# Kernel tuning notes

Hardware: AMD Instinct MI355X
Metric: run time of the kernel (lower is better)

Reference implementation:

```python
import jax, jax.numpy as jnp
import numpy as np

PSP_SIZES = (1, 3, 6, 8)  # KV length S = 1 + 9 + 36 + 64 = 110
BN_EPS = 1e-5


def conv1x1(x, W, b):
    # x: [B,C,H,W], W: [O,C], b: [O] -> [B,O,H,W]
    return jnp.einsum('bchw,oc->bohw', x, W) + b[None, :, None, None]


def psp(f):
    # f: [B,C,H,W] -> [B,C,S]; H,W divisible by all sizes so adaptive pool == block mean
    B, C, H, W = f.shape
    priors = []
    for s in PSP_SIZES:
        p = f.reshape(B, C, s, H // s, s, W // s).mean(axis=(3, 5))  # [B,C,s,s]
        priors.append(p.reshape(B, C, s * s))
    return jnp.concatenate(priors, axis=-1)  # [B,C,S]


def setup_inputs() -> dict:
    key = jax.random.key(0)
    ks = jax.random.split(key, 8)
    B, C, H, W = 8, 512, 72, 72
    Kc, Vc = 256, 256
    return {
        'x': jax.random.normal(ks[0], (B, C, H, W), jnp.float32),
        'Wk': jax.random.normal(ks[1], (Kc, C), jnp.float32) * (1.0 / np.sqrt(C)),
        'bk': jax.random.normal(ks[2], (Kc,), jnp.float32) * 0.01,
        'gamma': jnp.ones((Kc,), jnp.float32),
        'beta': jnp.zeros((Kc,), jnp.float32),
        'rmean': jnp.zeros((Kc,), jnp.float32),
        'rvar': jax.random.uniform(ks[3], (Kc,), jnp.float32, 0.5, 1.5),
        'Wv': jax.random.normal(ks[4], (Vc, C), jnp.float32) * (1.0 / np.sqrt(C)),
        'bv': jax.random.normal(ks[5], (Vc,), jnp.float32) * 0.01,
        'Ww': jax.random.normal(ks[6], (C, Vc), jnp.float32) * (1.0 / np.sqrt(Vc)),
        'bw': jnp.zeros((C,), jnp.float32),
    }


def reference(x, Wk, bk, gamma, beta, rmean, rvar, Wv, bv, Ww, bw):
    B, C, H, W = x.shape
    Kc = Wk.shape[0]
    Vc = Wv.shape[0]
    # f_value: conv1x1, then PSP -> value [B,S,Vc]
    value = psp(conv1x1(x, Wv, bv)).transpose(0, 2, 1)
    # f_key == f_query: conv1x1 + BN(inference) + ReLU
    k = conv1x1(x, Wk, bk)
    inv = gamma / jnp.sqrt(rvar + BN_EPS)
    k = jax.nn.relu(k * inv[None, :, None, None] + (beta - rmean * inv)[None, :, None, None])
    query = k.reshape(B, Kc, H * W).transpose(0, 2, 1)  # [B,HW,Kc]
    keyt = psp(k)  # [B,Kc,S]
    sim = jnp.einsum('bnk,bks->bns', query, keyt) * (Kc ** -0.5)
    sim = jax.nn.softmax(sim, axis=-1)
    context = jnp.einsum('bns,bsv->bnv', sim, value)  # [B,HW,Vc]
    context = context.transpose(0, 2, 1).reshape(B, Vc, H, W)
    return conv1x1(context, Ww, bw)
```

## Files before the change

kernel.cpp:

```cpp
#include <hip/hip_runtime.h>
#include <hip/hip_bf16.h>

#define HW    5184
#define WIDTH 72
#define CIN   512
#define KC    256
#define VC    256
#define NS    110
#define NSP   112
#define SPV   128
#define BATCH 8

typedef unsigned short u16;
typedef unsigned int   u32;
typedef __attribute__((ext_vector_type(8))) short bf16x8;
typedef __attribute__((ext_vector_type(4))) float f32x4;

typedef const __attribute__((address_space(1))) u32* gp_t;
typedef __attribute__((address_space(3))) u32* lp_t;

__device__ __forceinline__ u32 f2bf1(float f) {
    u32 u = __float_as_uint(f);
    return (u + 0x7FFFu + ((u >> 16) & 1u)) >> 16;
}
__device__ __forceinline__ u32 pack2(float a, float b) {
    return f2bf1(a) | (f2bf1(b) << 16);
}

__global__ void prep_kernel(const float* __restrict__ bk, const float* __restrict__ gamma,
                            const float* __restrict__ beta, const float* __restrict__ rmean,
                            const float* __restrict__ rvar, float* __restrict__ inv_out,
                            float* __restrict__ bc_out) {
    int i = threadIdx.x;
    float inv = gamma[i] * rsqrtf(rvar[i] + 1e-5f);
    inv_out[i] = inv;
    bc_out[i]  = bk[i] * inv + beta[i] - rmean[i] * inv;
}

__global__ __launch_bounds__(256) void cvt_w_kernel(
    const float* __restrict__ Wk, const float* __restrict__ Ww, const float* __restrict__ Wv,
    u16* __restrict__ Wkbf, u16* __restrict__ Wwbf, u16* __restrict__ Wvbf)
{
    int j = (blockIdx.x * 256 + threadIdx.x) * 4;
    const float* s; u16* d;
    if (j < KC * CIN)          { s = Wk; d = Wkbf; }
    else if (j < 2 * KC * CIN) { j -= KC * CIN;     s = Ww; d = Wwbf; }
    else                       { j -= 2 * KC * CIN; s = Wv; d = Wvbf; }
    float4 v = *(const float4*)&s[j];
    uint2 u;
    u.x = pack2(v.x, v.y);
    u.y = pack2(v.z, v.w);
    *(uint2*)&d[j] = u;
}

__global__ __launch_bounds__(256) void transpose_cvt_kernel(
    const float* __restrict__ in, u16* __restrict__ out, int C)
{
    const int z  = blockIdx.z;
    const int n0 = blockIdx.x * 32;
    const int k0 = blockIdx.y * 32;
    __shared__ float t[32][33];
    const int tx = threadIdx.x & 31, ty = threadIdx.x >> 5;
    const float* src = in + ((size_t)z * C + k0) * HW + n0;
#pragma unroll
    for (int i = 0; i < 4; i++)
        t[ty + i * 8][tx] = src[(size_t)(ty + i * 8) * HW + tx];
    __syncthreads();
    u16* dst = out + ((size_t)z * HW + n0) * C + k0;
    const int kp  = (threadIdx.x & 15) * 2;
    const int nl0 = threadIdx.x >> 4;
#pragma unroll
    for (int j = 0; j < 2; j++) {
        int nl = nl0 + j * 16;
        u32 u = pack2(t[kp][nl], t[kp + 1][nl]);
        *(u32*)&dst[(size_t)nl * C + kp] = u;
    }
}

__global__ __launch_bounds__(256) void gemm_nt_bf16(
    const u16* __restrict__ A, const u16* __restrict__ B, float* __restrict__ C,
    u16* __restrict__ Ct,
    int M, int N, int K, int nbx, int nby,
    const float* __restrict__ scale, const float* __restrict__ bias, int relu)
{
    const int tot = nbx * nby * BATCH;
    const int q = tot >> 3, r = tot & 7;
    const int xcd = blockIdx.x & 7;
    const int wg  = (xcd < r ? xcd * (q + 1) : r * (q + 1) + (xcd - r) * q) + (blockIdx.x >> 3);
    const int mb_ = wg % nby;
    const int nb_ = (wg / nby) % nbx;
    const int z   = wg / (nby * nbx);

    const int n0 = nb_ * 128;
    const int m0 = mb_ * 128;
    const size_t boff = (size_t)z * N * K;
    const size_t coff = (size_t)z * M * N;
    const int tid  = threadIdx.x;
    const int wid  = tid >> 6;
    const int lane = tid & 63;

    __shared__ __align__(16) u16 As[3][4][128][8];
    __shared__ __align__(16) u16 Bs[3][4][128][8];

    const int kg0  = (wid & 1) * 2;
    const int half = (wid >> 1) * 64;

    const u16* gA = A + (size_t)(m0 + half + lane) * K + kg0 * 8;
    int nIdx = n0 + half + lane;
    if (nIdx > N - 1) nIdx = N - 1;
    const u16* gB = B + boff + (size_t)nIdx * K + kg0 * 8;

    const int wm  = (wid >> 1) * 64;
    const int wn  = (wid & 1) * 64;
    const int l16 = lane & 15;
    const int lq  = lane >> 4;

    f32x4 acc[4][4];
#pragma unroll
    for (int mi = 0; mi < 4; mi++)
#pragma unroll
        for (int ni = 0; ni < 4; ni++)
            acc[mi][ni] = (f32x4){0.f, 0.f, 0.f, 0.f};

#define STAGE(d, kk)                                                                              \
    __builtin_amdgcn_global_load_lds((gp_t)(gA + (kk)),     (lp_t)&As[d][kg0][half][0], 16, 0, 0);\
    __builtin_amdgcn_global_load_lds((gp_t)(gA + (kk) + 8), (lp_t)&As[d][kg0+1][half][0],16, 0, 0);\
    __builtin_amdgcn_global_load_lds((gp_t)(gB + (kk)),     (lp_t)&Bs[d][kg0][half][0], 16, 0, 0);\
    __builtin_amdgcn_global_load_lds((gp_t)(gB + (kk) + 8), (lp_t)&Bs[d][kg0+1][half][0],16, 0, 0);

    const int NT = K >> 5;
    STAGE(0, 0)
    STAGE(1, 32)

    int cur = 0;
    for (int t = 0; t < NT; ++t) {
        if (t + 1 < NT) { asm volatile("s_waitcnt vmcnt(4)" ::: "memory"); }
        else            { asm volatile("s_waitcnt vmcnt(0)" ::: "memory"); }
        __builtin_amdgcn_s_barrier();
        __builtin_amdgcn_sched_barrier(0);

        if (t + 2 < NT) {
            int nb = cur + 2; if (nb >= 3) nb -= 3;
            STAGE(nb, (t + 2) * 32)
        }

        bf16x8 af[4], bf[4];
#pragma unroll
        for (int i = 0; i < 4; i++) {
            af[i] = *(const bf16x8*)&As[cur][lq][wm + i * 16 + l16][0];
            bf[i] = *(const bf16x8*)&Bs[cur][lq][wn + i * 16 + l16][0];
        }
        __builtin_amdgcn_s_setprio(1);
#pragma unroll
        for (int mi = 0; mi < 4; mi++)
#pragma unroll
            for (int ni = 0; ni < 4; ni++)
                acc[mi][ni] = __builtin_amdgcn_mfma_f32_16x16x32_bf16(
                    af[mi], bf[ni], acc[mi][ni], 0, 0, 0);
        __builtin_amdgcn_s_setprio(0);

        cur = (cur == 2) ? 0 : cur + 1;
    }
#undef STAGE

#pragma unroll
    for (int mi = 0; mi < 4; mi++) {
        const int mb = m0 + wm + mi * 16 + lq * 4;
        float sc[4], bi[4];
#pragma unroll
        for (int r2 = 0; r2 < 4; r2++) {
            sc[r2] = scale ? scale[mb + r2] : 1.0f;
            bi[r2] = bias  ? bias[mb + r2]  : 0.0f;
        }
#pragma unroll
        for (int ni = 0; ni < 4; ni++) {
            const int n = n0 + wn + ni * 16 + l16;
            if (n < N) {
                float v[4];
#pragma unroll
                for (int r2 = 0; r2 < 4; r2++) {
                    v[r2] = acc[mi][ni][r2] * sc[r2] + bi[r2];
                    if (relu) v[r2] = fmaxf(v[r2], 0.f);
                    C[coff + (size_t)(mb + r2) * N + n] = v[r2];
                }
                if (Ct) {
                    uint2 u;
                    u.x = pack2(v[0], v[1]);
                    u.y = pack2(v[2], v[3]);
                    *(uint2*)&Ct[(size_t)z * N * M + (size_t)n * M + mb] = u;
                }
            }
        }
    }
}

__global__ __launch_bounds__(256) void value_mfma_kernel(
    const u16* __restrict__ A, const u16* __restrict__ Bp,
    const float* __restrict__ bv, u16* __restrict__ valT)
{
    const int m0 = blockIdx.x * 128;
    const int b  = blockIdx.y;
    const int tid  = threadIdx.x;
    const int wid  = tid >> 6;
    const int lane = tid & 63;

    __shared__ __align__(16) u16 As[4][128][8];
    __shared__ __align__(16) u16 Bs[4][128][8];

    const int kg0  = (wid & 1) * 2;
    const int half = (wid >> 1) * 64;

    const u16* gA = A + (size_t)(m0 + half + lane) * CIN + kg0 * 8;
    const u16* gB = Bp + (size_t)b * SPV * CIN + (size_t)(half + lane) * CIN + kg0 * 8;

    lp_t lA0 = (lp_t)&As[kg0][half][0];
    lp_t lA1 = (lp_t)&As[kg0 + 1][half][0];
    lp_t lB0 = (lp_t)&Bs[kg0][half][0];
    lp_t lB1 = (lp_t)&Bs[kg0 + 1][half][0];

    const int wm  = (wid >> 1) * 64;
    const int wn  = (wid & 1) * 64;
    const int l16 = lane & 15;
    const int lq  = lane >> 4;

    f32x4 acc[4][4];
#pragma unroll
    for (int mi = 0; mi < 4; mi++)
#pragma unroll
        for (int ni = 0; ni < 4; ni++)
            acc[mi][ni] = (f32x4){0.f, 0.f, 0.f, 0.f};

    for (int k0 = 0; k0 < CIN; k0 += 32) {
        __builtin_amdgcn_global_load_lds((gp_t)(gA + k0),     lA0, 16, 0, 0);
        __builtin_amdgcn_global_load_lds((gp_t)(gA + k0 + 8), lA1, 16, 0, 0);
        __builtin_amdgcn_global_load_lds((gp_t)(gB + k0),     lB0, 16, 0, 0);
        __builtin_amdgcn_global_load_lds((gp_t)(gB + k0 + 8), lB1, 16, 0, 0);
        __syncthreads();

        bf16x8 af[4], bf[4];
#pragma unroll
        for (int i = 0; i < 4; i++) {
            af[i] = *(const bf16x8*)&As[lq][wm + i * 16 + l16][0];
            bf[i] = *(const bf16x8*)&Bs[lq][wn + i * 16 + l16][0];
        }
#pragma unroll
        for (int mi = 0; mi < 4; mi++)
#pragma unroll
            for (int ni = 0; ni < 4; ni++)
                acc[mi][ni] = __builtin_amdgcn_mfma_f32_16x16x32_bf16(
                    af[mi], bf[ni], acc[mi][ni], 0, 0, 0);
        __syncthreads();
    }

    char* vb = (char*)valT + (size_t)b * VC * SPV * 2;
#pragma unroll
    for (int mi = 0; mi < 4; mi++) {
        const int mb = m0 + wm + mi * 16 + lq * 4;
        float bi[4];
#pragma unroll
        for (int r = 0; r < 4; r++) bi[r] = bv[mb + r];
#pragma unroll
        for (int ni = 0; ni < 4; ni++) {
            const int n = wn + ni * 16 + l16;
#pragma unroll
            for (int r = 0; r < 4; r++) {
                const int v = mb + r;
                const int byte = v * 256 + ((n * 2) ^ ((v & 7) << 4));
                *(u16*)(vb + byte) = (u16)f2bf1(acc[mi][ni][r] + bi[r]);
            }
        }
    }
}

__global__ __launch_bounds__(128) void psp_pool_px_kernel(
    const float* __restrict__ in, u16* __restrict__ out)
{
    const int c = blockIdx.x;
    const int b = blockIdx.y;
    const int t = threadIdx.x;
    __shared__ float4 row4[1296];
    __shared__ float aux[100];
    float* row = (float*)row4;
    const float* src = in + ((size_t)b * CIN + c) * HW;
    for (int idx = t; idx < 1296; idx += 128)
        row4[idx] = *(const float4*)(src + idx * 4);
    __syncthreads();
    if (t < 64) {
        int r0 = (t >> 3) * 9, c0 = (t & 7) * 9;
        float s = 0.f;
        for (int i = 0; i < 9; i++)
            for (int j = 0; j < 9; j++) s += row[(r0 + i) * WIDTH + c0 + j];
        aux[t] = s;
    } else if (t < 100) {
        int tt = t - 64;
        int r0 = (tt / 6) * 12, c0 = (tt % 6) * 12;
        float s = 0.f;
        for (int i = 0; i < 12; i++)
            for (int j = 0; j < 12; j++) s += row[(r0 + i) * WIDTH + c0 + j];
        aux[64 + tt] = s;
    }
    __syncthreads();
    u16* ob = out + (size_t)b * SPV * CIN + c;
    if (t < 64) ob[(size_t)(46 + t) * CIN] = (u16)f2bf1(aux[t] * (1.f / 81.f));
    if (t < 36) ob[(size_t)(10 + t) * CIN] = (u16)f2bf1(aux[64 + t] * (1.f / 144.f));
    if (t < 9) {
        int r = t / 3, cc = t % 3;
        float s4 = aux[64 + (2 * r) * 6 + 2 * cc] + aux[64 + (2 * r) * 6 + 2 * cc + 1]
                 + aux[64 + (2 * r + 1) * 6 + 2 * cc] + aux[64 + (2 * r + 1) * 6 + 2 * cc + 1];
        ob[(size_t)(1 + t) * CIN] = (u16)f2bf1(s4 * (1.f / 576.f));
    }
    if (t == 0) {
        float s = 0.f;
        for (int i = 0; i < 64; i++) s += aux[i];
        ob[0] = (u16)f2bf1(s * (1.f / 5184.f));
    }
    if (t < 18) ob[(size_t)(110 + t) * CIN] = 0;
}

__global__ __launch_bounds__(128) void psp_pool_bf16_kernel(
    const float* __restrict__ in, u16* __restrict__ out)
{
    const int c = blockIdx.x;
    const int b = blockIdx.y;
    const int t = threadIdx.x;
    __shared__ float4 row4[1296];
    __shared__ float aux[100];
    float* row = (float*)row4;
    const float* src = in + ((size_t)b * KC + c) * HW;
    for (int idx = t; idx < 1296; idx += 128)
        row4[idx] = *(const float4*)(src + idx * 4);
    __syncthreads();
    if (t < 64) {
        int r0 = (t >> 3) * 9, c0 = (t & 7) * 9;
        float s = 0.f;
        for (int i = 0; i < 9; i++)
            for (int j = 0; j < 9; j++) s += row[(r0 + i) * WIDTH + c0 + j];
        aux[t] = s;
    } else if (t < 100) {
        int tt = t - 64;
        int r0 = (tt / 6) * 12, c0 = (tt % 6) * 12;
        float s = 0.f;
        for (int i = 0; i < 12; i++)
            for (int j = 0; j < 12; j++) s += row[(r0 + i) * WIDTH + c0 + j];
        aux[64 + tt] = s;
    }
    __syncthreads();
    char* ob = (char*)out + (size_t)b * NSP * KC * 2;
    const int c2 = c * 2;
#define KWR(S, V) *(u16*)(ob + (S) * 512 + (c2 ^ (((S) & 7) << 4))) = (u16)f2bf1(V)
    if (t < 64) KWR(46 + t, aux[t] * (1.f / 81.f));
    if (t < 36) KWR(10 + t, aux[64 + t] * (1.f / 144.f));
    if (t < 9) {
        int r = t / 3, cc = t % 3;
        float s4 = aux[64 + (2 * r) * 6 + 2 * cc] + aux[64 + (2 * r) * 6 + 2 * cc + 1]
                 + aux[64 + (2 * r + 1) * 6 + 2 * cc] + aux[64 + (2 * r + 1) * 6 + 2 * cc + 1];
        KWR(1 + t, s4 * (1.f / 576.f));
    }
    if (t == 0) {
        float s = 0.f;
        for (int i = 0; i < 64; i++) s += aux[i];
        KWR(0, s * (1.f / 5184.f));
        KWR(110, 0.f);
        KWR(111, 0.f);
    }
#undef KWR
}

__global__ __launch_bounds__(256) void attn_mfma_kernel(
    const u16* __restrict__ qT, const u16* __restrict__ keyt,
    const u16* __restrict__ valT, u16* __restrict__ ctxT)
{
    const int b    = blockIdx.y;
    const int tid  = threadIdx.x;
    const int wid  = tid >> 6;
    const int lane = tid & 63;
    const int l16  = lane & 15;
    const int lq   = lane >> 4;
    const int px0  = blockIdx.x * 64 + wid * 16;

    __shared__ __align__(16) u16 SM[61440];
    char* base = (char*)SM;
    const int VOFF = 57344;

    {
        const char* gk = (const char*)keyt + (size_t)b * (NSP * KC * 2);
        const char* gv = (const char*)valT + (size_t)b * (VC * SPV * 2);
#pragma unroll
        for (int i = 0; i < 14; i++) {
            const int o = (wid * 14 + i) * 1024;
            __builtin_amdgcn_global_load_lds((gp_t)(gk + o + lane * 16), (lp_t)(base + o), 16, 0, 0);
        }
#pragma unroll
        for (int i = 0; i < 16; i++) {
            const int o = (wid * 16 + i) * 1024;
            __builtin_amdgcn_global_load_lds((gp_t)(gv + o + lane * 16), (lp_t)(base + VOFF + o), 16, 0, 0);
        }
    }

    const u16* qrow = qT + ((size_t)b * HW + px0 + l16) * KC + lq * 8;
    bf16x8 aq[8];
#pragma unroll
    for (int ks = 0; ks < 8; ks++) aq[ks] = *(const bf16x8*)(qrow + ks * 32);

    __syncthreads();

    f32x4 acc[7];
#pragma unroll
    for (int ni = 0; ni < 7; ni++) acc[ni] = (f32x4){0.f, 0.f, 0.f, 0.f};
#pragma unroll
    for (int ks = 0; ks < 8; ks++) {
#pragma unroll
        for (int ni = 0; ni < 7; ni++) {
            const int s = ni * 16 + l16;
            const int byte = s * 512 + ((ks * 64 + lq * 16) ^ ((s & 7) << 4));
            bf16x8 bk = *(const bf16x8*)(base + byte);
            acc[ni] = __builtin_amdgcn_mfma_f32_16x16x32_bf16(aq[ks], bk, acc[ni], 0, 0, 0);
        }
    }

    if (l16 >= 14) acc[6] = (f32x4){-1e30f, -1e30f, -1e30f, -1e30f};

    float mx[4], sm[4], rn[4];
#pragma unroll
    for (int r = 0; r < 4; r++) {
        float m = acc[0][r];
#pragma unroll
        for (int ni = 1; ni < 7; ni++) m = fmaxf(m, acc[ni][r]);
        m = fmaxf(m, __shfl_xor(m, 1));
        m = fmaxf(m, __shfl_xor(m, 2));
        m = fmaxf(m, __shfl_xor(m, 4));
        m = fmaxf(m, __shfl_xor(m, 8));
        mx[r] = m * 0.0625f;
        sm[r] = 0.f;
    }

    __syncthreads();

    const int prow = wid * 16 + 4 * lq;
#pragma unroll
    for (int ni = 0; ni < 7; ni++) {
#pragma unroll
        for (int r = 0; r < 4; r++) {
            float p = __expf(acc[ni][r] * 0.0625f - mx[r]);
            sm[r] += p;
            const int row = prow + r;
            const int byte = row * 256 + (((ni * 16 + l16) * 2) ^ ((row & 7) << 4));
            *(u16*)(base + byte) = (u16)f2bf1(p);
        }
    }
    if (l16 < 2) {
#pragma unroll
        for (int r = 0; r < 4; r++) {
            const int row = prow + r;
            const int byte = row * 256 + ((224 + l16 * 16) ^ ((row & 7) << 4));
            *(bf16x8*)(base + byte) = (bf16x8){0, 0, 0, 0, 0, 0, 0, 0};
        }
    }
#pragma unroll
    for (int r = 0; r < 4; r++) {
        float s = sm[r];
        s += __shfl_xor(s, 1);
        s += __shfl_xor(s, 2);
        s += __shfl_xor(s, 4);
        s += __shfl_xor(s, 8);
        rn[r] = 1.f / s;
    }

    __syncthreads();

    f32x4 acc2[16];
#pragma unroll
    for (int ni = 0; ni < 16; ni++) acc2[ni] = (f32x4){0.f, 0.f, 0.f, 0.f};
    const int arow = wid * 16 + l16;
    const int aswz = (arow & 7) << 4;
#pragma unroll
    for (int ks = 0; ks < 4; ks++) {
        const int pbyte = arow * 256 + ((ks * 64 + lq * 16) ^ aswz);
        bf16x8 pa = *(const bf16x8*)(base + pbyte);
#pragma unroll
        for (int ni = 0; ni < 16; ni++) {
            const int v = ni * 16 + l16;
            const int vbyte = VOFF + v * 256 + ((ks * 64 + lq * 16) ^ ((v & 7) << 4));
            bf16x8 bvv = *(const bf16x8*)(base + vbyte);
            acc2[ni] = __builtin_amdgcn_mfma_f32_16x16x32_bf16(pa, bvv, acc2[ni], 0, 0, 0);
        }
    }

    u16* crow = ctxT + ((size_t)b * HW + px0 + 4 * lq) * VC + l16;
#pragma unroll
    for (int ni = 0; ni < 16; ni++) {
#pragma unroll
        for (int r = 0; r < 4; r++) {
            float v = acc2[ni][r] * rn[r];
            crow[(size_t)r * VC + ni * 16] = (u16)f2bf1(v);
        }
    }
}

extern "C" void kernel_launch(void* const* d_in, const int* in_sizes, int n_in,
                              void* d_out, int out_size, void* d_ws, size_t ws_size,
                              hipStream_t stream)
{
    const float* x     = (const float*)d_in[0];
    const float* Wk    = (const float*)d_in[1];
    const float* bk    = (const float*)d_in[2];
    const float* gamma = (const float*)d_in[3];
    const float* beta  = (const float*)d_in[4];
    const float* rmean = (const float*)d_in[5];
    const float* rvar  = (const float*)d_in[6];
    const float* Wv    = (const float*)d_in[7];
    const float* bv    = (const float*)d_in[8];
    const float* Ww    = (const float*)d_in[9];
    const float* bw    = (const float*)d_in[10];
    float* out = (float*)d_out;

    float* ws    = (float*)d_ws;
    float* k_ws  = ws;
    u16*   xT    = (u16*)(k_ws + (size_t)BATCH * KC * HW);
    u16*   ctxT  = xT;
    u16*   kT    = xT + (size_t)BATCH * HW * CIN;
    u16*   pxb   = kT + (size_t)BATCH * HW * KC;
    u16*   keytb = pxb + (size_t)BATCH * SPV * CIN;
    u16*   valT  = keytb + (size_t)BATCH * NSP * KC;
    u16*   Wkbf  = valT + (size_t)BATCH * VC * SPV;
    u16*   Wwbf  = Wkbf + (size_t)KC * CIN;
    u16*   Wvbf  = Wwbf + (size_t)CIN * VC;
    float* inv   = (float*)(Wvbf + (size_t)KC * CIN);
    float* bc    = inv + 256;

    prep_kernel<<<1, 256, 0, stream>>>(bk, gamma, beta, rmean, rvar, inv, bc);
    cvt_w_kernel<<<384, 256, 0, stream>>>(Wk, Ww, Wv, Wkbf, Wwbf, Wvbf);
    psp_pool_px_kernel<<<dim3(CIN, BATCH), 128, 0, stream>>>(x, pxb);
    transpose_cvt_kernel<<<dim3(HW / 32, CIN / 32, BATCH), 256, 0, stream>>>(x, xT, CIN);
    {
        const int nbx = (HW + 127) / 128, nby = KC / 128;
        gemm_nt_bf16<<<nbx * nby * BATCH, 256, 0, stream>>>(
            Wkbf, xT, k_ws, kT, KC, HW, CIN, nbx, nby, inv, bc, 1);
    }
    psp_pool_bf16_kernel<<<dim3(KC, BATCH), 128, 0, stream>>>(k_ws, keytb);
    value_mfma_kernel<<<dim3(2, BATCH), 256, 0, stream>>>(Wvbf, pxb, bv, valT);
    attn_mfma_kernel<<<dim3(HW / 64, BATCH), 256, 0, stream>>>(kT, keytb, valT, ctxT);
    {
        const int nbx = (HW + 127) / 128, nby = CIN / 128;
        gemm_nt_bf16<<<nbx * nby * BATCH, 256, 0, stream>>>(
            Wwbf, ctxT, out, nullptr, CIN, HW, VC, nbx, nby, nullptr, bw, 0);
    }
}
```

Before: 184.4 us.

## Fuse output 1x1 conv into attention kernel epilogue

The attention kernel now stages the normalized context tile for 64 pixels in shared memory as bf16 and multiplies it directly by Ww with MFMA, adding the bias and writing fp32 output. It staggers the stores through a swizzled per-wave scratch region so they coalesce. This removes the ctxT round-trip through global memory and one GEMM launch. In exchange, each block re-reads all of Ww from global/L2, holds 128 accumulator floats per lane (pressure on registers and occupancy), and writes only 64-pixel-wide output rows.

```diff
diff --git a/kernel.cpp b/kernel.cpp
--- a/kernel.cpp
+++ b/kernel.cpp
@@ -368,7 +368,8 @@
 
 __global__ __launch_bounds__(256) void attn_mfma_kernel(
     const u16* __restrict__ qT, const u16* __restrict__ keyt,
-    const u16* __restrict__ valT, u16* __restrict__ ctxT)
+    const u16* __restrict__ valT, const u16* __restrict__ Wwb,
+    const float* __restrict__ bw, float* __restrict__ out)
 {
     const int b    = blockIdx.y;
     const int tid  = threadIdx.x;
@@ -376,7 +377,8 @@
     const int lane = tid & 63;
     const int l16  = lane & 15;
     const int lq   = lane >> 4;
-    const int px0  = blockIdx.x * 64 + wid * 16;
+    const int nblk = blockIdx.x * 64;
+    const int px0  = nblk + wid * 16;
 
     __shared__ __align__(16) u16 SM[61440];
     char* base = (char*)SM;
@@ -417,7 +419,6 @@
             acc[ni] = __builtin_amdgcn_mfma_f32_16x16x32_bf16(aq[ks], bk, acc[ni], 0, 0, 0);
         }
     }
-
     if (l16 >= 14) acc[6] = (f32x4){-1e30f, -1e30f, -1e30f, -1e30f};
 
     float mx[4], sm[4], rn[4];
@@ -486,13 +487,76 @@
         }
     }
 
-    u16* crow = ctxT + ((size_t)b * HW + px0 + 4 * lq) * VC + l16;
+    __syncthreads();
+
 #pragma unroll
     for (int ni = 0; ni < 16; ni++) {
 #pragma unroll
         for (int r = 0; r < 4; r++) {
-            float v = acc2[ni][r] * rn[r];
-            crow[(size_t)r * VC + ni * 16] = (u16)f2bf1(v);
+            const int row = prow + r;
+            const int v = ni * 16 + l16;
+            const int byte = row * 512 + ((v * 2) ^ ((row & 7) << 4));
+            *(u16*)(base + byte) = (u16)f2bf1(acc2[ni][r] * rn[r]);
+        }
+    }
+    __syncthreads();
+
+    const int wc0 = wid * 128;
+    f32x4 accg[4][8];
+#pragma unroll
+    for (int pi = 0; pi < 4; pi++)
+#pragma unroll
+        for (int cj = 0; cj < 8; cj++)
+            accg[pi][cj] = (f32x4){0.f, 0.f, 0.f, 0.f};
+
+    const u16* wwbase = Wwb + (size_t)(wc0 + l16) * VC + lq * 8;
+#pragma unroll
+    for (int ks = 0; ks < 8; ks++) {
+        bf16x8 af[4];
+#pragma unroll
+        for (int pi = 0; pi < 4; pi++) {
+            const int px = pi * 16 + l16;
+            const int byte = px * 512 + ((ks * 64 + lq * 16) ^ ((px & 7) << 4));
+            af[pi] = *(const bf16x8*)(base + byte);
+        }
+        bf16x8 bfr[8];
+#pragma unroll
+        for (int cj = 0; cj < 8; cj++)
+            bfr[cj] = *(const bf16x8*)(wwbase + (size_t)cj * 16 * VC + ks * 32);
+#pragma unroll
+        for (int pi = 0; pi < 4; pi++)
+#pragma unroll
+            for (int cj = 0; cj < 8; cj++)
+                accg[pi][cj] = __builtin_amdgcn_mfma_f32_16x16x32_bf16(
+                    af[pi], bfr[cj], accg[pi][cj], 0, 0, 0);
+    }
+
+    char* scr = base + VOFF + wid * 16384;
+    float* outb = out + (size_t)b * CIN * HW + nblk;
+#pragma unroll
+    for (int ci = 0; ci < 4; ci++) {
+#pragma unroll
+        for (int cjh = 0; cjh < 2; cjh++) {
+            const int cj = ci * 2 + cjh;
+            const int cl = cjh * 16 + l16;
+            const int swz = (cl & 7) << 5;
+#pragma unroll
+            for (int pi = 0; pi < 4; pi++)
+#pragma unroll
+                for (int r = 0; r < 4; r++) {
+                    const int px = pi * 16 + 4 * lq + r;
+                    *(float*)(scr + cl * 256 + ((px * 4) ^ swz)) = accg[pi][cj][r];
+                }
+        }
+#pragma unroll
+        for (int cr = 0; cr < 8; cr++) {
+            const int cl = cr * 4 + lq;
+            const int swz = (cl & 7) << 5;
+            float4 vv = *(const float4*)(scr + cl * 256 + ((l16 * 16) ^ swz));
+            const int c = wc0 + ci * 32 + cl;
+            const float bb = bw[c];
+            vv.x += bb; vv.y += bb; vv.z += bb; vv.w += bb;
+            *(float4*)&outb[(size_t)c * HW + l16 * 4] = vv;
         }
     }
 }
@@ -517,7 +581,6 @@
     float* ws    = (float*)d_ws;
     float* k_ws  = ws;
     u16*   xT    = (u16*)(k_ws + (size_t)BATCH * KC * HW);
-    u16*   ctxT  = xT;
     u16*   kT    = xT + (size_t)BATCH * HW * CIN;
     u16*   pxb   = kT + (size_t)BATCH * HW * KC;
     u16*   keytb = pxb + (size_t)BATCH * SPV * CIN;
@@ -539,10 +602,6 @@
     }
     psp_pool_bf16_kernel<<<dim3(KC, BATCH), 128, 0, stream>>>(k_ws, keytb);
     value_mfma_kernel<<<dim3(2, BATCH), 256, 0, stream>>>(Wvbf, pxb, bv, valT);
-    attn_mfma_kernel<<<dim3(HW / 64, BATCH), 256, 0, stream>>>(kT, keytb, valT, ctxT);
-    {
-        const int nbx = (HW + 127) / 128, nby = CIN / 128;
-        gemm_nt_bf16<<<nbx * nby * BATCH, 256, 0, stream>>>(
-            Wwbf, ctxT, out, nullptr, CIN, HW, VC, nbx, nby, nullptr, bw, 0);
-    }
-}
+    attn_mfma_kernel<<<dim3(HW / 64, BATCH), 256, 0, stream>>>(
+        kT, keytb, valT, Wwbf, bw, out);
+}
```

After: 178.1 us. 1.04x faster.
